# Optimization experiments

Hardware: AMD Instinct MI355X
Metric: run time of the kernel (lower is better)

## Reference

```python
import jax, jax.numpy as jnp
import numpy as np

B, S, D, H = 64, 2048, 64, 128  # batch, seq_len, input_dim, rnn_hidden_dim


def setup_inputs() -> dict:
    key = jax.random.key(0)
    k = jax.random.split(key, 6)
    x = jax.random.normal(k[0], (B, S, D), dtype=jnp.float32)
    # LSTM params, keras gate order: i, f, g(candidate), o
    Wx = jax.random.normal(k[1], (D, 4 * H), dtype=jnp.float32) / np.sqrt(D)
    Wh = jax.random.normal(k[2], (H, 4 * H), dtype=jnp.float32) / np.sqrt(H)
    b = jnp.zeros((4 * H,), dtype=jnp.float32).at[H:2 * H].set(1.0)  # unit_forget_bias
    # Dense(1, sigmoid) head
    Wd = jax.random.normal(k[3], (H, 1), dtype=jnp.float32) / np.sqrt(H)
    bd = jnp.zeros((1,), dtype=jnp.float32)
    return {"x": x, "Wx": Wx, "Wh": Wh, "b": b, "Wd": Wd, "bd": bd}


def _lstm_seq(x, Wx, Wh, b):
    H_ = Wh.shape[0]
    # precompute input projections for all timesteps: [B,S,4H]
    xz = jnp.einsum('bsd,dg->bsg', x, Wx) + b

    def step(carry, xz_t):
        h, c = carry
        z = xz_t + h @ Wh  # [B,4H]
        i = jax.nn.sigmoid(z[:, :H_])
        f = jax.nn.sigmoid(z[:, H_:2 * H_])
        g = jnp.tanh(z[:, 2 * H_:3 * H_])
        o = jax.nn.sigmoid(z[:, 3 * H_:])
        c = f * c + i * g
        h = o * jnp.tanh(c)
        return (h, c), h

    h0 = jnp.zeros((x.shape[0], H_), dtype=x.dtype)
    c0 = jnp.zeros((x.shape[0], H_), dtype=x.dtype)
    _, hs = jax.lax.scan(step, (h0, c0), jnp.swapaxes(xz, 0, 1))  # hs: [S,B,H]
    return jnp.swapaxes(hs, 0, 1)  # [B,S,H]


def reference(x, Wx, Wh, b, Wd, bd):
    h = _lstm_seq(x, Wx, Wh, b)                 # [B,S,H]
    return jax.nn.sigmoid(h @ Wd + bd)          # [B,S,1]
```

## Files before the change

### kernel.cpp

```cpp
#include <hip/hip_runtime.h>

#define B_ 64
#define S_ 2048
#define D_ 64
#define H_ 128
#define G_ 512
#define CH 16

typedef float f32x4 __attribute__((ext_vector_type(4)));
typedef short bf16x8 __attribute__((ext_vector_type(8)));

#define MFMA16(a, b, c) __builtin_amdgcn_mfma_f32_16x16x32_bf16((a), (b), (c), 0, 0, 0)

#if __has_builtin(__builtin_amdgcn_exp2f)
#define EXP2(x) __builtin_amdgcn_exp2f(x)
#else
#define EXP2(x) exp2f(x)
#endif
#define RCPF(x) __builtin_amdgcn_rcpf(x)

#define LOG2E 1.442695041f

__device__ __forceinline__ short f2bf(float f) {
    unsigned u = __builtin_bit_cast(unsigned, f);
    return (short)((u + 0x7FFFu + ((u >> 16) & 1u)) >> 16);
}
__device__ __forceinline__ float bflo(unsigned u) { return __builtin_bit_cast(float, u << 16); }
__device__ __forceinline__ float bfhi(unsigned u) { return __builtin_bit_cast(float, u & 0xFFFF0000u); }
__device__ __forceinline__ float sigm_f(float x) { return RCPF(1.0f + EXP2(x * -LOG2E)); }

__launch_bounds__(512, 2)
__global__ void lstm_fused(const float* __restrict__ x, const float* __restrict__ Wx,
                           const float* __restrict__ Wh, const float* __restrict__ bias,
                           const float* __restrict__ Wd, const float* __restrict__ bd,
                           float* __restrict__ out) {
    const int tid = threadIdx.x;
    const int lane = tid & 63;
    const int wid = tid >> 6;
    const int l15 = lane & 15;
    const int l4 = lane >> 4;
    const int bb = blockIdx.x;

    __shared__ alignas(16) short hist[CH][H_];
    __shared__ alignas(16) short xbf[CH][72];
    __shared__ float xzc[CH][G_];

    ((unsigned*)hist)[tid] = 0u;
    ((unsigned*)hist)[tid + 512] = 0u;

    const int col0 = wid * 16 + l15;
    const bool b0 = (l4 & 1) != 0;
    const bool b1 = (l4 & 2) != 0;

    bf16x8 bh[4][4];
#pragma unroll
    for (int ct = 0; ct < 4; ++ct) {
        const int col = ct * H_ + col0;
#pragma unroll
        for (int kt = 0; kt < 4; ++kt) {
            bf16x8 v;
#pragma unroll
            for (int e = 0; e < 8; ++e)
                v[e] = f2bf(Wh[(kt * 32 + l4 * 8 + e) * G_ + col]);
            bh[ct][kt] = v;
        }
    }
    bf16x8 bx[4][2];
#pragma unroll
    for (int ct = 0; ct < 4; ++ct) {
        const int col = ct * H_ + col0;
#pragma unroll
        for (int kt = 0; kt < 2; ++kt) {
            bf16x8 v;
#pragma unroll
            for (int e = 0; e < 8; ++e)
                v[e] = f2bf(Wx[(kt * 32 + l4 * 8 + e) * G_ + col]);
            bx[ct][kt] = v;
        }
    }

    float bvr[4];
#pragma unroll
    for (int ct = 0; ct < 4; ++ct) bvr[ct] = bias[ct * H_ + col0];
    const float wd0 = Wd[lane * 2 + 0];
    const float wd1 = Wd[lane * 2 + 1];
    const float bdv = bd[0];
    float c_reg = 0.0f;

    const float m_c = (l4 == 2) ? (-2.0f * LOG2E) : (-LOG2E);
    const float a_c = (l4 == 2) ? 2.0f : 1.0f;
    const float b_c = (l4 == 2) ? -1.0f : 0.0f;

    const float* xb = x + (size_t)bb * S_ * D_;
    float* ob = out + (size_t)bb * S_;

    float xp0 = xb[tid * 2 + 0];
    float xp1 = xb[tid * 2 + 1];

    for (int tc = 0; tc < S_; tc += CH) {
        xbf[tid >> 5][(tid & 31) * 2 + 0] = f2bf(xp0);
        xbf[tid >> 5][(tid & 31) * 2 + 1] = f2bf(xp1);
        __syncthreads();
        if (tc + CH < S_) {
            xp0 = xb[(tc + CH) * D_ + tid * 2 + 0];
            xp1 = xb[(tc + CH) * D_ + tid * 2 + 1];
        }
#pragma unroll
        for (int ct = 0; ct < 4; ++ct) {
            f32x4 acc = {bvr[ct], bvr[ct], bvr[ct], bvr[ct]};
#pragma unroll
            for (int kt = 0; kt < 2; ++kt) {
                const bf16x8 a = *reinterpret_cast<const bf16x8*>(&xbf[l15][kt * 32 + l4 * 8]);
                acc = MFMA16(a, bx[ct][kt], acc);
            }
#pragma unroll
            for (int r = 0; r < 4; ++r)
                xzc[l4 * 4 + r][col0 * 4 + ct] = acc[r];
        }
        if (tc > 0) {
#pragma unroll
            for (int s = 0; s < 2; ++s) {
                const int row = wid * 2 + s;
                const unsigned hp = *reinterpret_cast<const unsigned*>(&hist[row][lane * 2]);
                float p = bflo(hp) * wd0 + bfhi(hp) * wd1;
                p += __shfl_xor(p, 1);  p += __shfl_xor(p, 2);  p += __shfl_xor(p, 4);
                p += __shfl_xor(p, 8);  p += __shfl_xor(p, 16); p += __shfl_xor(p, 32);
                if (lane == 0) ob[tc - CH + row] = sigm_f(p + bdv);
            }
        }
        __syncthreads();

#pragma unroll
        for (int tm = 0; tm < CH; ++tm) {
            const int prev = (tm + CH - 1) & (CH - 1);
            const short* hsrc = hist[prev];
            const bf16x8 a0 = *reinterpret_cast<const bf16x8*>(&hsrc[ 0 + l4 * 8]);
            const bf16x8 a1 = *reinterpret_cast<const bf16x8*>(&hsrc[32 + l4 * 8]);
            const bf16x8 a2 = *reinterpret_cast<const bf16x8*>(&hsrc[64 + l4 * 8]);
            const bf16x8 a3 = *reinterpret_cast<const bf16x8*>(&hsrc[96 + l4 * 8]);
            const float xz1 = xzc[tm][col0 * 4 + l4];

            const f32x4 zz = {0.f, 0.f, 0.f, 0.f};
            f32x4 acc0 = zz, acc1 = zz, acc2 = zz, acc3 = zz;
            acc0 = MFMA16(a0, bh[0][0], acc0);
            acc1 = MFMA16(a0, bh[1][0], acc1);
            acc2 = MFMA16(a0, bh[2][0], acc2);
            acc3 = MFMA16(a0, bh[3][0], acc3);
            acc0 = MFMA16(a1, bh[0][1], acc0);
            acc1 = MFMA16(a1, bh[1][1], acc1);
            acc2 = MFMA16(a1, bh[2][1], acc2);
            acc3 = MFMA16(a1, bh[3][1], acc3);
            acc0 = MFMA16(a2, bh[0][2], acc0);
            acc1 = MFMA16(a2, bh[1][2], acc1);
            acc2 = MFMA16(a2, bh[2][2], acc2);
            acc3 = MFMA16(a2, bh[3][2], acc3);
            acc0 = MFMA16(a3, bh[0][3], acc0);
            acc1 = MFMA16(a3, bh[1][3], acc1);
            acc2 = MFMA16(a3, bh[2][3], acc2);
            acc3 = MFMA16(a3, bh[3][3], acc3);

            float zsel = b1 ? (b0 ? acc3[0] : acc2[0]) : (b0 ? acc1[0] : acc0[0]);
            zsel += xz1;

            const float t = a_c * RCPF(1.0f + EXP2(zsel * m_c)) + b_c;

            const float r1 = __shfl_xor(t, 16);
            const float r2 = __shfl_xor(t, 32);
            const float r3 = __shfl_xor(r2, 16);
            const float iv = b1 ? (b0 ? r3 : r2) : (b0 ? r1 : t);
            const float fv = b1 ? (b0 ? r2 : r3) : (b0 ? t  : r1);
            const float gv = b1 ? (b0 ? r1 : t ) : (b0 ? r3 : r2);
            const float ov = b1 ? (b0 ? t  : r1) : (b0 ? r2 : r3);

            c_reg = fv * c_reg + iv * gv;
            const float th = 2.0f * RCPF(1.0f + EXP2(c_reg * (-2.0f * LOG2E))) - 1.0f;
            const float hv = ov * th;

            unsigned hb;
            asm("v_cvt_pk_bf16_f32 %0, %1, %2" : "=v"(hb) : "v"(hv), "v"(0.0f));
            if (lane < 16) hist[tm][col0] = (short)hb;
            __syncthreads();
        }
    }

#pragma unroll
    for (int s = 0; s < 2; ++s) {
        const int row = wid * 2 + s;
        const unsigned hp = *reinterpret_cast<const unsigned*>(&hist[row][lane * 2]);
        float p = bflo(hp) * wd0 + bfhi(hp) * wd1;
        p += __shfl_xor(p, 1);  p += __shfl_xor(p, 2);  p += __shfl_xor(p, 4);
        p += __shfl_xor(p, 8);  p += __shfl_xor(p, 16); p += __shfl_xor(p, 32);
        if (lane == 0) ob[S_ - CH + row] = sigm_f(p + bdv);
    }
}

extern "C" void kernel_launch(void* const* d_in, const int* in_sizes, int n_in,
                              void* d_out, int out_size, void* d_ws, size_t ws_size,
                              hipStream_t stream) {
    const float* x  = (const float*)d_in[0];
    const float* Wx = (const float*)d_in[1];
    const float* Wh = (const float*)d_in[2];
    const float* b  = (const float*)d_in[3];
    const float* Wd = (const float*)d_in[4];
    const float* bd = (const float*)d_in[5];
    float* out = (float*)d_out;

    lstm_fused<<<B_, 512, 0, stream>>>(x, Wx, Wh, b, Wd, bd, out);
}
```

Baseline: 1.067 ms.

## Fold input projection into MFMA accumulator and restrict cell update to one lane group

Each step now loads the four precomputed input-projection values as one vector read and seeds the MFMA accumulators with them, so the separate add after the matmul goes away. The gate exchange drops from four conditional selects to three direct xor shuffles. Only lanes 0-15 compute the cell and hidden update. The per-step barrier becomes a manual lgkmcnt wait plus s_barrier fenced by sched_barrier. Seeding only element 0 of each accumulator leaves elements 1-3 holding stale values from the previous step, which is safe only because those elements are never read.

```diff
diff --git a/kernel.cpp b/kernel.cpp
--- a/kernel.cpp
+++ b/kernel.cpp
@@ -11,15 +11,15 @@
 typedef short bf16x8 __attribute__((ext_vector_type(8)));
 
 #define MFMA16(a, b, c) __builtin_amdgcn_mfma_f32_16x16x32_bf16((a), (b), (c), 0, 0, 0)
-
-#if __has_builtin(__builtin_amdgcn_exp2f)
-#define EXP2(x) __builtin_amdgcn_exp2f(x)
-#else
-#define EXP2(x) exp2f(x)
-#endif
 #define RCPF(x) __builtin_amdgcn_rcpf(x)
-
 #define LOG2E 1.442695041f
+
+#define STEP_SYNC() do {                                  \
+    __builtin_amdgcn_sched_barrier(0);                    \
+    asm volatile("s_waitcnt lgkmcnt(0)" ::: "memory");    \
+    __builtin_amdgcn_s_barrier();                         \
+    __builtin_amdgcn_sched_barrier(0);                    \
+} while (0)
 
 __device__ __forceinline__ short f2bf(float f) {
     unsigned u = __builtin_bit_cast(unsigned, f);
@@ -27,7 +27,7 @@
 }
 __device__ __forceinline__ float bflo(unsigned u) { return __builtin_bit_cast(float, u << 16); }
 __device__ __forceinline__ float bfhi(unsigned u) { return __builtin_bit_cast(float, u & 0xFFFF0000u); }
-__device__ __forceinline__ float sigm_f(float x) { return RCPF(1.0f + EXP2(x * -LOG2E)); }
+__device__ __forceinline__ float sigm_f(float x) { return RCPF(1.0f + __expf(-x)); }
 
 __launch_bounds__(512, 2)
 __global__ void lstm_fused(const float* __restrict__ x, const float* __restrict__ Wx,
@@ -43,7 +43,7 @@
 
     __shared__ alignas(16) short hist[CH][H_];
     __shared__ alignas(16) short xbf[CH][72];
-    __shared__ float xzc[CH][G_];
+    __shared__ alignas(16) float xzc[CH][G_];
 
     ((unsigned*)hist)[tid] = 0u;
     ((unsigned*)hist)[tid + 512] = 0u;
@@ -96,6 +96,8 @@
 
     float xp0 = xb[tid * 2 + 0];
     float xp1 = xb[tid * 2 + 1];
+
+    f32x4 acc0 = {0.f, 0.f, 0.f, 0.f}, acc1 = acc0, acc2 = acc0, acc3 = acc0;
 
     for (int tc = 0; tc < S_; tc += CH) {
         xbf[tid >> 5][(tid & 31) * 2 + 0] = f2bf(xp0);
@@ -107,15 +109,15 @@
         }
 #pragma unroll
         for (int ct = 0; ct < 4; ++ct) {
-            f32x4 acc = {bvr[ct], bvr[ct], bvr[ct], bvr[ct]};
+            f32x4 cacc = {bvr[ct], bvr[ct], bvr[ct], bvr[ct]};
 #pragma unroll
             for (int kt = 0; kt < 2; ++kt) {
                 const bf16x8 a = *reinterpret_cast<const bf16x8*>(&xbf[l15][kt * 32 + l4 * 8]);
-                acc = MFMA16(a, bx[ct][kt], acc);
+                cacc = MFMA16(a, bx[ct][kt], cacc);
             }
 #pragma unroll
             for (int r = 0; r < 4; ++r)
-                xzc[l4 * 4 + r][col0 * 4 + ct] = acc[r];
+                xzc[l4 * 4 + r][col0 * 4 + ct] = cacc[r];
         }
         if (tc > 0) {
 #pragma unroll
@@ -138,10 +140,10 @@
             const bf16x8 a1 = *reinterpret_cast<const bf16x8*>(&hsrc[32 + l4 * 8]);
             const bf16x8 a2 = *reinterpret_cast<const bf16x8*>(&hsrc[64 + l4 * 8]);
             const bf16x8 a3 = *reinterpret_cast<const bf16x8*>(&hsrc[96 + l4 * 8]);
-            const float xz1 = xzc[tm][col0 * 4 + l4];
-
-            const f32x4 zz = {0.f, 0.f, 0.f, 0.f};
-            f32x4 acc0 = zz, acc1 = zz, acc2 = zz, acc3 = zz;
+            const f32x4 xzq = *reinterpret_cast<const f32x4*>(&xzc[tm][col0 * 4]);
+
+            acc0[0] = xzq[0];  acc1[0] = xzq[1];  acc2[0] = xzq[2];  acc3[0] = xzq[3];
+
             acc0 = MFMA16(a0, bh[0][0], acc0);
             acc1 = MFMA16(a0, bh[1][0], acc1);
             acc2 = MFMA16(a0, bh[2][0], acc2);
@@ -159,27 +161,21 @@
             acc2 = MFMA16(a3, bh[2][3], acc2);
             acc3 = MFMA16(a3, bh[3][3], acc3);
 
-            float zsel = b1 ? (b0 ? acc3[0] : acc2[0]) : (b0 ? acc1[0] : acc0[0]);
-            zsel += xz1;
-
-            const float t = a_c * RCPF(1.0f + EXP2(zsel * m_c)) + b_c;
-
-            const float r1 = __shfl_xor(t, 16);
-            const float r2 = __shfl_xor(t, 32);
-            const float r3 = __shfl_xor(r2, 16);
-            const float iv = b1 ? (b0 ? r3 : r2) : (b0 ? r1 : t);
-            const float fv = b1 ? (b0 ? r2 : r3) : (b0 ? t  : r1);
-            const float gv = b1 ? (b0 ? r1 : t ) : (b0 ? r3 : r2);
-            const float ov = b1 ? (b0 ? t  : r1) : (b0 ? r2 : r3);
-
-            c_reg = fv * c_reg + iv * gv;
-            const float th = 2.0f * RCPF(1.0f + EXP2(c_reg * (-2.0f * LOG2E))) - 1.0f;
-            const float hv = ov * th;
-
-            unsigned hb;
-            asm("v_cvt_pk_bf16_f32 %0, %1, %2" : "=v"(hb) : "v"(hv), "v"(0.0f));
-            if (lane < 16) hist[tm][col0] = (short)hb;
-            __syncthreads();
+            const float zsel = b1 ? (b0 ? acc3[0] : acc2[0]) : (b0 ? acc1[0] : acc0[0]);
+
+            const float t = a_c * RCPF(1.0f + __expf(zsel * m_c * 0.693147181f)) + b_c;
+
+            const float rf = __shfl_xor(t, 16);
+            const float rg = __shfl_xor(t, 32);
+            const float ro = __shfl_xor(t, 48);
+
+            if (lane < 16) {
+                c_reg = rf * c_reg + t * rg;
+                const float th = 2.0f * RCPF(1.0f + __expf(-2.0f * c_reg)) - 1.0f;
+                const float hv = ro * th;
+                hist[tm][col0] = f2bf(hv);
+            }
+            STEP_SYNC();
         }
     }
 
```

After: 1.118 ms. +4.8%, slower.
